# Optimization experiments

Measured on AMD Instinct MI355X. Metric: run time of the kernel, lower is better.

The kernel has to match this reference:

```python
import jax, jax.numpy as jnp
import numpy as np
import math

N_HEADS = 4
GELU = lambda x: jax.nn.gelu(x, approximate=False)  # torch nn.GELU default = exact erf

def _ln(x, s, b):
    m = jnp.mean(x, axis=-1, keepdims=True)
    v = jnp.mean((x - m) ** 2, axis=-1, keepdims=True)
    return (x - m) * jax.lax.rsqrt(v + 1e-5) * s + b

def _fwd(materials, in_seq, proj_vars, param_vars, enc_w1, enc_b1, enc_w2, enc_b2, sos,
         tl_wq, tl_wk, tl_wv, tl_bq, tl_bk, tl_bv, tl_wo, tl_bo,
         tl_ln1s, tl_ln1b, tl_ln2s, tl_ln2b, tl_fw1, tl_fb1, tl_fw2, tl_fb2,
         pw1, pb1, pw2, pb2, pw3, pb3, pw4, pb4, pw5, pb5,
         ipw1, ipb1, ipw2, ipb2, hw1, hb1, hw2, hb2, hw3, hb3):
    B = in_seq.shape[0]
    # encoder input MLP: [B,S,1] -> [B,S,D]
    x = GELU(in_seq @ enc_w1 + enc_b1) @ enc_w2 + enc_b2
    x = jnp.concatenate([jnp.broadcast_to(sos, (B, 1, sos.shape[-1])), x], axis=1)
    S1, D = x.shape[1], x.shape[2]
    dh = D // N_HEADS
    # sinusoidal positional encoding
    pos = jnp.arange(S1, dtype=jnp.float32)[:, None]
    div = jnp.exp(jnp.arange(0, D, 2, dtype=jnp.float32) * (-math.log(10000.0) / D))
    ang = pos * div
    pe = jnp.stack([jnp.sin(ang), jnp.cos(ang)], axis=-1).reshape(S1, D)
    x = x + pe
    scale = 1.0 / math.sqrt(dh)
    # post-LN TransformerEncoder layers (torch default norm_first=False), eval mode (no dropout)
    for l in range(tl_wq.shape[0]):
        q = (x @ tl_wq[l] + tl_bq[l]).reshape(B, S1, N_HEADS, dh).transpose(0, 2, 1, 3)
        k = (x @ tl_wk[l] + tl_bk[l]).reshape(B, S1, N_HEADS, dh).transpose(0, 2, 1, 3)
        v = (x @ tl_wv[l] + tl_bv[l]).reshape(B, S1, N_HEADS, dh).transpose(0, 2, 1, 3)
        att = jax.nn.softmax(jnp.einsum('bhqd,bhkd->bhqk', q, k) * scale, axis=-1)
        o = jnp.einsum('bhqk,bhkd->bhqd', att, v).transpose(0, 2, 1, 3).reshape(B, S1, D)
        x = _ln(x + o @ tl_wo[l] + tl_bo[l], tl_ln1s[l], tl_ln1b[l])
        f = GELU(x @ tl_fw1[l] + tl_fb1[l]) @ tl_fw2[l] + tl_fb2[l]
        x = _ln(x + f, tl_ln2s[l], tl_ln2b[l])
    sos_out = x[:, 0]
    h = jnp.concatenate([proj_vars, sos_out], axis=1)
    for w, b in ((pw1, pb1), (pw2, pb2), (pw3, pb3), (pw4, pb4)):
        h = GELU(h @ w + b)
    proj_out = h @ pw5 + pb5
    pp = GELU(param_vars @ ipw1 + ipb1) @ ipw2 + ipb2
    mi = jnp.concatenate([pp, proj_out], axis=1)  # [B, output_features+param_vars]
    # MaterialHead mask-gather-MLP-scatter == run every tiny head densely, pick by material id
    h1 = GELU(jnp.einsum('bi,mio->mbo', mi, hw1) + hb1[:, None, :])
    h2 = GELU(jnp.einsum('mbi,mio->mbo', h1, hw2) + hb2[:, None, :])
    h3 = jnp.einsum('mbi,mio->mbo', h2, hw3) + hb3[:, None, :]  # [M,B,1]
    return h3[materials, jnp.arange(B)]  # [B,1]

def setup_inputs() -> dict:
    key = jax.random.key(0)
    ks = iter(jax.random.split(key, 64))
    def rn(shape, scale=0.05):
        return jax.random.normal(next(ks), shape, dtype=jnp.float32) * scale
    B, S, IN, EL, D, L, DFF = 64, 1024, 1, 48, 64, 3, 256
    PV, PP, OF, M = 3, 3, 24, 3
    IF = OF + PP
    return dict(
        in_seq=rn((B, S, IN), 1.0),
        proj_vars=rn((B, PV), 1.0),
        param_vars=rn((B, PP), 1.0),
        materials=jax.random.randint(next(ks), (B,), 0, M),
        enc_w1=rn((IN, EL)), enc_b1=rn((EL,)), enc_w2=rn((EL, D)), enc_b2=rn((D,)),
        sos=rn((1, 1, D)),
        tl_wq=rn((L, D, D)), tl_wk=rn((L, D, D)), tl_wv=rn((L, D, D)),
        tl_bq=rn((L, D)), tl_bk=rn((L, D)), tl_bv=rn((L, D)),
        tl_wo=rn((L, D, D)), tl_bo=rn((L, D)),
        tl_ln1s=jnp.ones((L, D)), tl_ln1b=jnp.zeros((L, D)),
        tl_ln2s=jnp.ones((L, D)), tl_ln2b=jnp.zeros((L, D)),
        tl_fw1=rn((L, D, DFF)), tl_fb1=rn((L, DFF)), tl_fw2=rn((L, DFF, D)), tl_fb2=rn((L, D)),
        pw1=rn((PV + D, 34)), pb1=rn((34,)), pw2=rn((34, 11)), pb2=rn((11,)),
        pw3=rn((11, 36)), pb3=rn((36,)), pw4=rn((36, 22)), pb4=rn((22,)),
        pw5=rn((22, OF)), pb5=rn((OF,)),
        ipw1=rn((PP, 3)), ipb1=rn((3,)), ipw2=rn((3, PP)), ipb2=rn((PP,)),
        hw1=rn((M, IF, 15)), hb1=rn((M, 15)), hw2=rn((M, 15, 18)), hb2=rn((M, 18)),
        hw3=rn((M, 18, 1)), hb3=rn((M, 1)),
    )

def reference(in_seq, proj_vars, param_vars, materials, enc_w1, enc_b1, enc_w2, enc_b2, sos,
              tl_wq, tl_wk, tl_wv, tl_bq, tl_bk, tl_bv, tl_wo, tl_bo,
              tl_ln1s, tl_ln1b, tl_ln2s, tl_ln2b, tl_fw1, tl_fb1, tl_fw2, tl_fb2,
              pw1, pb1, pw2, pb2, pw3, pb3, pw4, pb4, pw5, pb5,
              ipw1, ipb1, ipw2, ipb2, hw1, hb1, hw2, hb2, hw3, hb3):
    return _fwd(materials, in_seq, proj_vars, param_vars, enc_w1, enc_b1, enc_w2, enc_b2, sos,
                tl_wq, tl_wk, tl_wv, tl_bq, tl_bk, tl_bv, tl_wo, tl_bo,
                tl_ln1s, tl_ln1b, tl_ln2s, tl_ln2b, tl_fw1, tl_fb1, tl_fw2, tl_fb2,
                pw1, pb1, pw2, pb2, pw3, pb3, pw4, pb4, pw5, pb5,
                ipw1, ipb1, ipw2, ipb2, hw1, hb1, hw2, hb2, hw3, hb3)
```

## Files before the change

kernel.cpp:

```cpp
#include <hip/hip_runtime.h>
#include <hip/hip_bf16.h>
#include <math.h>

#define BB   64
#define SS   1024
#define S1C  1025
#define DD   64
#define NHD  4
#define NBH  (BB * NHD)
#define DHD  16
#define DFFC 256
#define NLAY 3
#define NTOK (BB * S1C)
#define SPAD 1056
#define TGRP2 9
#define FTT   16
#define FT2   32
#define HPAD 264
#define OPAD 68
#define YPAD 72
#define QSCL 0.36067376022224085f

typedef const float* fp;
typedef __attribute__((ext_vector_type(8))) short bf16x8;
typedef __attribute__((ext_vector_type(4))) float f32x4;

#if __has_builtin(__builtin_amdgcn_exp2f)
#define RAW_EXP2(x) __builtin_amdgcn_exp2f(x)
#else
#define RAW_EXP2(x) __expf(0.6931471805599453f * (x))
#endif
#if __has_builtin(__builtin_amdgcn_rcpf)
#define RAW_RCP(x) __builtin_amdgcn_rcpf(x)
#else
#define RAW_RCP(x) (1.0f / (x))
#endif

__device__ __forceinline__ float gelu_exact(float x) {
    return 0.5f * x * (1.0f + erff(x * 0.7071067811865475f));
}
__device__ __forceinline__ float erf_fast(float x) {
    float ax = fabsf(x);
    float t = RAW_RCP(1.0f + 0.3275911f * ax);
    float p = t * (0.254829592f + t * (-0.284496736f + t * (1.421413741f +
              t * (-1.453152027f + t * 1.061405429f))));
    float e = RAW_EXP2(ax * ax * -1.4426950408889634f);
    float r = 1.0f - p * e;
    return copysignf(r, x);
}
__device__ __forceinline__ float gelu_fast(float x) {
    return 0.5f * x * (1.0f + erf_fast(x * 0.7071067811865475f));
}
__device__ __forceinline__ short f2b(float f) {
    unsigned u = __float_as_uint(f);
    return (short)((u + 0x7fffu + ((u >> 16) & 1u)) >> 16);
}
__device__ __forceinline__ short f2b_pos(float f) {
    return (short)((__float_as_uint(f) + 0x8000u) >> 16);
}

__global__ __launch_bounds__(256) void k_wconv(
    fp wq, fp wk, fp wv, fp wo, fp w1, fp w2,
    short* __restrict__ wqkvT, short* __restrict__ woT,
    short* __restrict__ w1T, short* __restrict__ w2T)
{
    int l = blockIdx.y;
    int i = blockIdx.x * 256 + threadIdx.x;
    if (i < 12288) {
        int p = i >> 12, rem = i & 4095;
        int d = rem >> 6, j = rem & 63;
        fp src = (p == 0 ? wq : p == 1 ? wk : wv) + (size_t)l * 4096;
        float v = src[j * 64 + d];
        if (p == 0) v *= QSCL;
        wqkvT[(size_t)l * 12288 + i] = f2b(v);
    } else if (i < 16384) {
        int rem = i - 12288;
        woT[(size_t)l * 4096 + rem] = f2b(wo[(size_t)l * 4096 + (rem & 63) * 64 + (rem >> 6)]);
    } else if (i < 32768) {
        int rem = i - 16384;
        w1T[(size_t)l * 16384 + rem] = f2b(w1[(size_t)l * 16384 + (rem & 63) * 256 + (rem >> 6)]);
    } else {
        int rem = i - 32768;
        w2T[(size_t)l * 16384 + rem] = f2b(w2[(size_t)l * 16384 + (rem & 255) * 64 + (rem >> 8)]);
    }
}

__global__ __launch_bounds__(64) void k_zero(
    short* __restrict__ qb, short* __restrict__ kb, short* __restrict__ vbt)
{
    int bh = blockIdx.x, t = threadIdx.x;
    for (int i = t; i < 31 * 16; i += 64) {
        int r = i >> 4, c = i & 15;
        size_t idx = ((size_t)bh * SPAD + 1025 + r) * 16 + c;
        qb[idx] = 0; kb[idx] = 0;
    }
    for (int i = t; i < 16 * 31; i += 64) {
        int e = i / 31, c = i % 31;
        vbt[((size_t)bh * 16 + e) * SPAD + 1025 + c] = 0;
    }
}

__global__ __launch_bounds__(256) void k_encode(
    fp in_seq, fp enc_w1, fp enc_b1, fp enc_w2, fp enc_b2, fp sos,
    float* __restrict__ x, short* __restrict__ xb)
{
    int t = threadIdx.x;
    int w = t >> 6, d = t & 63;
    int tok = blockIdx.x * 4 + w;
    int b = tok / S1C, s = tok % S1C;
    __shared__ float e[4][48];
    float val;
    if (s == 0) {
        val = sos[d];
    } else {
        float tin = in_seq[b * SS + (s - 1)];
        if (d < 48) e[w][d] = gelu_fast(tin * enc_w1[d] + enc_b1[d]);
        float acc = enc_b2[d];
        for (int j = 0; j < 48; ++j) acc += e[w][j] * enc_w2[j * DD + d];
        val = acc;
    }
    int i2 = (d >> 1) * 2;
    float factor = RAW_EXP2((float)i2 * (-9.210340371976184f / 64.0f) * 1.4426950408889634f);
    float ang = (float)s * factor;
    val += (d & 1) ? __cosf(ang) : __sinf(ang);
    x[(size_t)tok * DD + d] = val;
    xb[(size_t)tok * DD + d] = f2b(val);
}

__global__ __launch_bounds__(256) void k_qkv(
    const short* __restrict__ xb, const short* __restrict__ wqkvT,
    fp bq, fp bk, fp bv,
    short* __restrict__ qb, short* __restrict__ kb, short* __restrict__ vbt)
{
    int blk = blockIdx.x, t = threadIdx.x;
    int tok0 = blk * FTT;
    int w = t >> 6, l = t & 63;
    int quad = l >> 4, lo = l & 15;

    bf16x8 a0 = *(const bf16x8*)(xb + ((size_t)(tok0 + lo)) * DD + quad * 8);
    bf16x8 a1 = *(const bf16x8*)(xb + ((size_t)(tok0 + lo)) * DD + 32 + quad * 8);

    int tokr[4], br[4], sr[4];
    #pragma unroll
    for (int r = 0; r < 4; ++r) {
        tokr[r] = tok0 + quad * 4 + r;
        br[r] = tokr[r] / S1C; sr[r] = tokr[r] % S1C;
    }

    int n = w * 16 + lo;
    #pragma unroll
    for (int p = 0; p < 3; ++p) {
        const short* wT = wqkvT + (size_t)p * 4096 + (size_t)n * 64;
        bf16x8 b0 = *(const bf16x8*)(wT + quad * 8);
        bf16x8 b1 = *(const bf16x8*)(wT + 32 + quad * 8);
        f32x4 c = __builtin_amdgcn_mfma_f32_16x16x32_bf16(a0, b0, (f32x4){0,0,0,0}, 0, 0, 0);
        c = __builtin_amdgcn_mfma_f32_16x16x32_bf16(a1, b1, c, 0, 0, 0);
        float bias = (p == 0) ? bq[n] * QSCL : (p == 1) ? bk[n] : bv[n];
        #pragma unroll
        for (int r = 0; r < 4; ++r) {
            int bh = br[r] * NHD + w;
            short val = f2b(c[r] + bias);
            if (p == 0)      qb[((size_t)bh * SPAD + sr[r]) * 16 + lo] = val;
            else if (p == 1) kb[((size_t)bh * SPAD + sr[r]) * 16 + lo] = val;
            else             vbt[((size_t)bh * 16 + lo) * SPAD + sr[r]] = val;
        }
    }
}

__global__ __launch_bounds__(256) void k_attn(
    const short* __restrict__ qb, const short* __restrict__ kb,
    const short* __restrict__ vbt, short* __restrict__ ob)
{
    int bid = blockIdx.x;
    int bh  = bid % NBH;
    int grp = bid / NBH;
    int b = bh >> 2, h = bh & 3;
    int t = threadIdx.x;
    int w = t >> 6, l = t & 63;
    int quad = l >> 4, lo = l & 15;
    int t0 = grp * 4 + w;
    int t1 = t0 + 36;
    if (t1 > 65) t1 = 65;
    int qg0 = t0 * 16, qg1 = t1 * 16;

    __shared__ short pt_all[4][2][16][40];
    short (*pt0)[40] = pt_all[w][0];
    short (*pt1)[40] = pt_all[w][1];

    const short* qbase = qb + (size_t)bh * SPAD * 16;
    const short* kbase = kb + (size_t)bh * SPAD * 16;
    const short* vbase = vbt + (size_t)bh * 16 * SPAD;

    bf16x8 aQ0 = {0,0,0,0,0,0,0,0}, aQ1 = {0,0,0,0,0,0,0,0};
    if (quad < 2) {
        aQ0 = *(const bf16x8*)(qbase + ((size_t)(qg0 + lo)) * 16 + quad * 8);
        aQ1 = *(const bf16x8*)(qbase + ((size_t)(qg1 + lo)) * 16 + quad * 8);
    }

    const short ONE = 0x3F80;
    bf16x8 aOne = {ONE, ONE, ONE, ONE, ONE, ONE, ONE, ONE};

    f32x4 oc0 = {0.f,0.f,0.f,0.f}, oc1 = {0.f,0.f,0.f,0.f};
    f32x4 dn0 = {0.f,0.f,0.f,0.f}, dn1 = {0.f,0.f,0.f,0.f};

    for (int ch = 0; ch < 32; ++ch) {
        #pragma unroll
        for (int t01 = 0; t01 < 2; ++t01) {
            int krow = ch * 32 + t01 * 16 + lo;
            bf16x8 bK = *(const bf16x8*)(kbase + (size_t)krow * 16 + (quad & 1) * 8);
            f32x4 c0 = __builtin_amdgcn_mfma_f32_16x16x32_bf16(
                aQ0, bK, (f32x4){0.f,0.f,0.f,0.f}, 0, 0, 0);
            f32x4 c1 = __builtin_amdgcn_mfma_f32_16x16x32_bf16(
                aQ1, bK, (f32x4){0.f,0.f,0.f,0.f}, 0, 0, 0);
            #pragma unroll
            for (int r = 0; r < 4; ++r) {
                pt0[quad * 4 + r][t01 * 16 + lo] = f2b_pos(RAW_EXP2(c0[r]));
                pt1[quad * 4 + r][t01 * 16 + lo] = f2b_pos(RAW_EXP2(c1[r]));
            }
        }
        bf16x8 aV = *(const bf16x8*)(vbase + (size_t)lo * SPAD + ch * 32 + quad * 8);
        bf16x8 pB0 = *(const bf16x8*)&pt0[lo][quad * 8];
        oc0 = __builtin_amdgcn_mfma_f32_16x16x32_bf16(aV, pB0, oc0, 0, 0, 0);
        dn0 = __builtin_amdgcn_mfma_f32_16x16x32_bf16(aOne, pB0, dn0, 0, 0, 0);
        bf16x8 pB1 = *(const bf16x8*)&pt1[lo][quad * 8];
        oc1 = __builtin_amdgcn_mfma_f32_16x16x32_bf16(aV, pB1, oc1, 0, 0, 0);
        dn1 = __builtin_amdgcn_mfma_f32_16x16x32_bf16(aOne, pB1, dn1, 0, 0, 0);
    }
    {
        #pragma unroll
        for (int t01 = 0; t01 < 2; ++t01) {
            int krow = 1024 + t01 * 16 + lo;
            bf16x8 bK = *(const bf16x8*)(kbase + (size_t)krow * 16 + (quad & 1) * 8);
            f32x4 c0 = __builtin_amdgcn_mfma_f32_16x16x32_bf16(
                aQ0, bK, (f32x4){0.f,0.f,0.f,0.f}, 0, 0, 0);
            f32x4 c1 = __builtin_amdgcn_mfma_f32_16x16x32_bf16(
                aQ1, bK, (f32x4){0.f,0.f,0.f,0.f}, 0, 0, 0);
            bool valid = (krow <= 1024);
            #pragma unroll
            for (int r = 0; r < 4; ++r) {
                pt0[quad * 4 + r][t01 * 16 + lo] = f2b_pos(valid ? RAW_EXP2(c0[r]) : 0.f);
                pt1[quad * 4 + r][t01 * 16 + lo] = f2b_pos(valid ? RAW_EXP2(c1[r]) : 0.f);
            }
        }
        bf16x8 aV = *(const bf16x8*)(vbase + (size_t)lo * SPAD + 1024 + quad * 8);
        bf16x8 pB0 = *(const bf16x8*)&pt0[lo][quad * 8];
        oc0 = __builtin_amdgcn_mfma_f32_16x16x32_bf16(aV, pB0, oc0, 0, 0, 0);
        dn0 = __builtin_amdgcn_mfma_f32_16x16x32_bf16(aOne, pB0, dn0, 0, 0, 0);
        bf16x8 pB1 = *(const bf16x8*)&pt1[lo][quad * 8];
        oc1 = __builtin_amdgcn_mfma_f32_16x16x32_bf16(aV, pB1, oc1, 0, 0, 0);
        dn1 = __builtin_amdgcn_mfma_f32_16x16x32_bf16(aOne, pB1, dn1, 0, 0, 0);
    }

    {
        int qrow = qg0 + lo;
        if (qrow < S1C) {
            float inv = 1.0f / dn0[0];
            unsigned p0 = (unsigned short)f2b(oc0[0] * inv) | ((unsigned)(unsigned short)f2b(oc0[1] * inv) << 16);
            unsigned p1 = (unsigned short)f2b(oc0[2] * inv) | ((unsigned)(unsigned short)f2b(oc0[3] * inv) << 16);
            *(uint2*)(ob + ((size_t)b * S1C + qrow) * DD + h * DHD + quad * 4) = make_uint2(p0, p1);
        }
    }
    {
        int qrow = qg1 + lo;
        if (qrow < S1C) {
            float inv = 1.0f / dn1[0];
            unsigned p0 = (unsigned short)f2b(oc1[0] * inv) | ((unsigned)(unsigned short)f2b(oc1[1] * inv) << 16);
            unsigned p1 = (unsigned short)f2b(oc1[2] * inv) | ((unsigned)(unsigned short)f2b(oc1[3] * inv) << 16);
            *(uint2*)(ob + ((size_t)b * S1C + qrow) * DD + h * DHD + quad * 4) = make_uint2(p0, p1);
        }
    }
}

__global__ __launch_bounds__(256) void k_block(
    const short* __restrict__ ob, float* __restrict__ x,
    const short* __restrict__ woT, fp bo, fp ln1s, fp ln1b,
    const short* __restrict__ w1T, fp b1, const short* __restrict__ w2T, fp b2,
    fp ln2s, fp ln2b,
    const short* __restrict__ wqkvTn, fp bqn, fp bkn, fp bvn,
    short* __restrict__ qb, short* __restrict__ kb, short* __restrict__ vbt,
    int has_next)
{
    int blk = blockIdx.x, t = threadIdx.x;
    int tok0 = blk * FT2;
    int w = t >> 6, l = t & 63;
    int quad = l >> 4, lo = l & 15;

    __shared__ float otf[FT2][OPAD];
    __shared__ short ys[FT2][YPAD];
    __shared__ short hid[FT2][HPAD];

    {
        const short* obp0 = ob + ((size_t)(tok0 + lo)) * DD;
        const short* obp1 = ob + ((size_t)(tok0 + 16 + lo)) * DD;
        bf16x8 a0 = *(const bf16x8*)(obp0 + quad * 8);
        bf16x8 a1 = *(const bf16x8*)(obp0 + 32 + quad * 8);
        bf16x8 a2 = *(const bf16x8*)(obp1 + quad * 8);
        bf16x8 a3 = *(const bf16x8*)(obp1 + 32 + quad * 8);
        int n = w * 16 + lo;
        const short* wT = woT + (size_t)n * 64;
        bf16x8 b0 = *(const bf16x8*)(wT + quad * 8);
        bf16x8 bb = *(const bf16x8*)(wT + 32 + quad * 8);
        f32x4 c0 = __builtin_amdgcn_mfma_f32_16x16x32_bf16(a0, b0, (f32x4){0,0,0,0}, 0, 0, 0);
        c0 = __builtin_amdgcn_mfma_f32_16x16x32_bf16(a1, bb, c0, 0, 0, 0);
        f32x4 c1 = __builtin_amdgcn_mfma_f32_16x16x32_bf16(a2, b0, (f32x4){0,0,0,0}, 0, 0, 0);
        c1 = __builtin_amdgcn_mfma_f32_16x16x32_bf16(a3, bb, c1, 0, 0, 0);
        float bov = bo[n];
        #pragma unroll
        for (int r = 0; r < 4; ++r) {
            otf[quad * 4 + r][n] = c0[r] + bov;
            otf[16 + quad * 4 + r][n] = c1[r] + bov;
        }
    }
    __syncthreads();

    int d = l;
    float yv[8];
    {
        float s1 = ln1s[d], bl1 = ln1b[d];
        #pragma unroll
        for (int i = 0; i < 8; ++i) {
            int tt = w * 8 + i;
            float val = otf[tt][d] + x[(size_t)(tok0 + tt) * DD + d];
            float sum = val, vs = val * val;
            #pragma unroll
            for (int off = 32; off > 0; off >>= 1) {
                sum += __shfl_xor(sum, off, 64);
                vs  += __shfl_xor(vs, off, 64);
            }
            float mean = sum * (1.0f / 64.0f);
            float var = vs * (1.0f / 64.0f) - mean * mean;
            float y = (val - mean) * rsqrtf(var + 1e-5f) * s1 + bl1;
            yv[i] = y;
            ys[tt][d] = f2b(y);
        }
    }
    __syncthreads();

    {
        bf16x8 a0 = *(const bf16x8*)&ys[lo][quad * 8];
        bf16x8 a1 = *(const bf16x8*)&ys[lo][32 + quad * 8];
        bf16x8 a2 = *(const bf16x8*)&ys[16 + lo][quad * 8];
        bf16x8 a3 = *(const bf16x8*)&ys[16 + lo][32 + quad * 8];
        #pragma unroll
        for (int i = 0; i < 4; ++i) {
            int n = w * 64 + i * 16 + lo;
            const short* wT = w1T + (size_t)n * 64;
            bf16x8 b0 = *(const bf16x8*)(wT + quad * 8);
            bf16x8 bb = *(const bf16x8*)(wT + 32 + quad * 8);
            f32x4 c0 = __builtin_amdgcn_mfma_f32_16x16x32_bf16(a0, b0, (f32x4){0,0,0,0}, 0, 0, 0);
            c0 = __builtin_amdgcn_mfma_f32_16x16x32_bf16(a1, bb, c0, 0, 0, 0);
            f32x4 c1 = __builtin_amdgcn_mfma_f32_16x16x32_bf16(a2, b0, (f32x4){0,0,0,0}, 0, 0, 0);
            c1 = __builtin_amdgcn_mfma_f32_16x16x32_bf16(a3, bb, c1, 0, 0, 0);
            float b1v = b1[n];
            #pragma unroll
            for (int r = 0; r < 4; ++r) {
                hid[quad * 4 + r][n] = f2b(gelu_fast(c0[r] + b1v));
                hid[16 + quad * 4 + r][n] = f2b(gelu_fast(c1[r] + b1v));
            }
        }
    }
    __syncthreads();

    {
        f32x4 c20 = {0.f,0.f,0.f,0.f}, c21 = {0.f,0.f,0.f,0.f};
        const short* wT2 = w2T + (size_t)(w * 16 + lo) * 256;
        #pragma unroll
        for (int kc = 0; kc < 8; ++kc) {
            bf16x8 b2f = *(const bf16x8*)(wT2 + kc * 32 + quad * 8);
            bf16x8 a20 = *(const bf16x8*)&hid[lo][kc * 32 + quad * 8];
            bf16x8 a21 = *(const bf16x8*)&hid[16 + lo][kc * 32 + quad * 8];
            c20 = __builtin_amdgcn_mfma_f32_16x16x32_bf16(a20, b2f, c20, 0, 0, 0);
            c21 = __builtin_amdgcn_mfma_f32_16x16x32_bf16(a21, b2f, c21, 0, 0, 0);
        }
        float b2v = b2[w * 16 + lo];
        #pragma unroll
        for (int r = 0; r < 4; ++r) {
            otf[quad * 4 + r][w * 16 + lo] = c20[r] + b2v;
            otf[16 + quad * 4 + r][w * 16 + lo] = c21[r] + b2v;
        }
    }
    __syncthreads();

    {
        float s2 = ln2s[d], bl2 = ln2b[d];
        #pragma unroll
        for (int i = 0; i < 8; ++i) {
            int tt = w * 8 + i;
            float val = otf[tt][d] + yv[i];
            float sum = val, vs = val * val;
            #pragma unroll
            for (int off = 32; off > 0; off >>= 1) {
                sum += __shfl_xor(sum, off, 64);
                vs  += __shfl_xor(vs, off, 64);
            }
            float mean = sum * (1.0f / 64.0f);
            float var = vs * (1.0f / 64.0f) - mean * mean;
            float y = (val - mean) * rsqrtf(var + 1e-5f) * s2 + bl2;
            x[(size_t)(tok0 + tt) * DD + d] = y;
            ys[tt][d] = f2b(y);
        }
    }
    __syncthreads();

    if (has_next) {
        bf16x8 a0 = *(const bf16x8*)&ys[lo][quad * 8];
        bf16x8 a1 = *(const bf16x8*)&ys[lo][32 + quad * 8];
        bf16x8 a2 = *(const bf16x8*)&ys[16 + lo][quad * 8];
        bf16x8 a3 = *(const bf16x8*)&ys[16 + lo][32 + quad * 8];
        int n = w * 16 + lo;
        #pragma unroll
        for (int p = 0; p < 3; ++p) {
            const short* wT = wqkvTn + (size_t)p * 4096 + (size_t)n * 64;
            bf16x8 b0 = *(const bf16x8*)(wT + quad * 8);
            bf16x8 bb = *(const bf16x8*)(wT + 32 + quad * 8);
            f32x4 c0 = __builtin_amdgcn_mfma_f32_16x16x32_bf16(a0, b0, (f32x4){0,0,0,0}, 0, 0, 0);
            c0 = __builtin_amdgcn_mfma_f32_16x16x32_bf16(a1, bb, c0, 0, 0, 0);
            f32x4 c1 = __builtin_amdgcn_mfma_f32_16x16x32_bf16(a2, b0, (f32x4){0,0,0,0}, 0, 0, 0);
            c1 = __builtin_amdgcn_mfma_f32_16x16x32_bf16(a3, bb, c1, 0, 0, 0);
            float bias = (p == 0) ? bqn[n] * QSCL : (p == 1) ? bkn[n] : bvn[n];
            #pragma unroll
            for (int r = 0; r < 4; ++r) {
                int tok = tok0 + quad * 4 + r;
                int bb0 = tok / S1C, ss0 = tok % S1C;
                int bh = bb0 * NHD + w;
                short val = f2b(c0[r] + bias);
                int tok2 = tok + 16;
                int bb1 = tok2 / S1C, ss1 = tok2 % S1C;
                int bh2 = bb1 * NHD + w;
                short val2 = f2b(c1[r] + bias);
                if (p == 0) {
                    qb[((size_t)bh * SPAD + ss0) * 16 + lo] = val;
                    qb[((size_t)bh2 * SPAD + ss1) * 16 + lo] = val2;
                } else if (p == 1) {
                    kb[((size_t)bh * SPAD + ss0) * 16 + lo] = val;
                    kb[((size_t)bh2 * SPAD + ss1) * 16 + lo] = val2;
                } else {
                    vbt[((size_t)bh * 16 + lo) * SPAD + ss0] = val;
                    vbt[((size_t)bh2 * 16 + lo) * SPAD + ss1] = val2;
                }
            }
        }
    }
}

__global__ __launch_bounds__(64) void k_head(
    const float* __restrict__ x, fp proj_vars, fp param_vars,
    const int* __restrict__ materials,
    fp pw1, fp pb1, fp pw2, fp pb2, fp pw3, fp pb3,
    fp pw4, fp pb4, fp pw5, fp pb5,
    fp ipw1, fp ipb1, fp ipw2, fp ipb2,
    fp hw1, fp hb1, fp hw2, fp hb2, fp hw3, fp hb3,
    float* __restrict__ out)
{
    int b = blockIdx.x;
    int tid = threadIdx.x;
    __shared__ float A[80], Bf[80], pp[8], mi[32];

    if (tid < 3) A[tid] = proj_vars[b * 3 + tid];
    A[3 + tid] = x[((size_t)b * S1C + 0) * DD + tid];
    __syncthreads();

    if (tid < 34) {
        float a = pb1[tid];
        for (int i = 0; i < 67; ++i) a += A[i] * pw1[i * 34 + tid];
        Bf[tid] = gelu_exact(a);
    }
    __syncthreads();
    if (tid < 11) {
        float a = pb2[tid];
        for (int i = 0; i < 34; ++i) a += Bf[i] * pw2[i * 11 + tid];
        A[tid] = gelu_exact(a);
    }
    __syncthreads();
    if (tid < 36) {
        float a = pb3[tid];
        for (int i = 0; i < 11; ++i) a += A[i] * pw3[i * 36 + tid];
        Bf[tid] = gelu_exact(a);
    }
    __syncthreads();
    if (tid < 22) {
        float a = pb4[tid];
        for (int i = 0; i < 36; ++i) a += Bf[i] * pw4[i * 22 + tid];
        A[tid] = gelu_exact(a);
    }
    __syncthreads();
    if (tid < 24) {
        float a = pb5[tid];
        for (int i = 0; i < 22; ++i) a += A[i] * pw5[i * 24 + tid];
        mi[3 + tid] = a;
    }
    if (tid < 3) {
        float a = ipb1[tid];
        for (int i = 0; i < 3; ++i) a += param_vars[b * 3 + i] * ipw1[i * 3 + tid];
        pp[tid] = gelu_exact(a);
    }
    __syncthreads();
    if (tid < 3) {
        float a = ipb2[tid];
        for (int i = 0; i < 3; ++i) a += pp[i] * ipw2[i * 3 + tid];
        mi[tid] = a;
    }
    __syncthreads();

    int m = materials[b];
    if (tid < 15) {
        float a = hb1[m * 15 + tid];
        for (int i = 0; i < 27; ++i) a += mi[i] * hw1[(m * 27 + i) * 15 + tid];
        A[tid] = gelu_exact(a);
    }
    __syncthreads();
    if (tid < 18) {
        float a = hb2[m * 18 + tid];
        for (int i = 0; i < 15; ++i) a += A[i] * hw2[(m * 15 + i) * 18 + tid];
        Bf[tid] = gelu_exact(a);
    }
    __syncthreads();
    if (tid == 0) {
        float a = hb3[m];
        for (int i = 0; i < 18; ++i) a += Bf[i] * hw3[m * 18 + i];
        out[b] = a;
    }
}

extern "C" void kernel_launch(void* const* d_in, const int* in_sizes, int n_in,
                              void* d_out, int out_size, void* d_ws, size_t ws_size,
                              hipStream_t stream) {
    fp in_seq     = (fp)d_in[0];
    fp proj_vars  = (fp)d_in[1];
    fp param_vars = (fp)d_in[2];
    const int* materials = (const int*)d_in[3];
    fp enc_w1 = (fp)d_in[4];
    fp enc_b1 = (fp)d_in[5];
    fp enc_w2 = (fp)d_in[6];
    fp enc_b2 = (fp)d_in[7];
    fp sos    = (fp)d_in[8];
    fp tl_wq  = (fp)d_in[9];
    fp tl_wk  = (fp)d_in[10];
    fp tl_wv  = (fp)d_in[11];
    fp tl_bq  = (fp)d_in[12];
    fp tl_bk  = (fp)d_in[13];
    fp tl_bv  = (fp)d_in[14];
    fp tl_wo  = (fp)d_in[15];
    fp tl_bo  = (fp)d_in[16];
    fp tl_ln1s = (fp)d_in[17];
    fp tl_ln1b = (fp)d_in[18];
    fp tl_ln2s = (fp)d_in[19];
    fp tl_ln2b = (fp)d_in[20];
    fp tl_fw1 = (fp)d_in[21];
    fp tl_fb1 = (fp)d_in[22];
    fp tl_fw2 = (fp)d_in[23];
    fp tl_fb2 = (fp)d_in[24];
    fp pw1 = (fp)d_in[25]; fp pb1 = (fp)d_in[26];
    fp pw2 = (fp)d_in[27]; fp pb2 = (fp)d_in[28];
    fp pw3 = (fp)d_in[29]; fp pb3 = (fp)d_in[30];
    fp pw4 = (fp)d_in[31]; fp pb4 = (fp)d_in[32];
    fp pw5 = (fp)d_in[33]; fp pb5 = (fp)d_in[34];
    fp ipw1 = (fp)d_in[35]; fp ipb1 = (fp)d_in[36];
    fp ipw2 = (fp)d_in[37]; fp ipb2 = (fp)d_in[38];
    fp hw1 = (fp)d_in[39]; fp hb1 = (fp)d_in[40];
    fp hw2 = (fp)d_in[41]; fp hb2 = (fp)d_in[42];
    fp hw3 = (fp)d_in[43]; fp hb3 = (fp)d_in[44];

    float* x  = (float*)d_ws;
    short* ob = (short*)(x + (size_t)NTOK * DD);
    short* xb = ob + (size_t)NTOK * DD;
    short* qb = xb + (size_t)NTOK * DD;
    short* kb = qb + (size_t)NBH * SPAD * 16;
    short* vbt = kb + (size_t)NBH * SPAD * 16;
    short* wqkvT = vbt + (size_t)NBH * 16 * SPAD;
    short* woT = wqkvT + (size_t)NLAY * 12288;
    short* w1T = woT + (size_t)NLAY * 4096;
    short* w2T = w1T + (size_t)NLAY * 16384;

    k_wconv<<<dim3(192, NLAY), 256, 0, stream>>>(
        tl_wq, tl_wk, tl_wv, tl_wo, tl_fw1, tl_fw2, wqkvT, woT, w1T, w2T);
    k_zero<<<NBH, 64, 0, stream>>>(qb, kb, vbt);
    k_encode<<<NTOK / 4, 256, 0, stream>>>(in_seq, enc_w1, enc_b1, enc_w2, enc_b2, sos, x, xb);

    k_qkv<<<NTOK / FTT, 256, 0, stream>>>(
        xb, wqkvT,
        tl_bq, tl_bk, tl_bv,
        qb, kb, vbt);

    for (int l = 0; l < NLAY; ++l) {
        k_attn<<<NBH * TGRP2, 256, 0, stream>>>(qb, kb, vbt, ob);
        int ln = (l + 1 < NLAY) ? (l + 1) : l;
        k_block<<<NTOK / FT2, 256, 0, stream>>>(
            ob, x,
            woT + (size_t)l * 4096, tl_bo + (size_t)l * DD,
            tl_ln1s + (size_t)l * DD, tl_ln1b + (size_t)l * DD,
            w1T + (size_t)l * 16384, tl_fb1 + (size_t)l * DFFC,
            w2T + (size_t)l * 16384, tl_fb2 + (size_t)l * DD,
            tl_ln2s + (size_t)l * DD, tl_ln2b + (size_t)l * DD,
            wqkvT + (size_t)ln * 12288,
            tl_bq + (size_t)ln * DD, tl_bk + (size_t)ln * DD, tl_bv + (size_t)ln * DD,
            qb, kb, vbt,
            (l + 1 < NLAY) ? 1 : 0);
    }

    k_head<<<BB, 64, 0, stream>>>(
        x, proj_vars, param_vars, materials,
        pw1, pb1, pw2, pb2, pw3, pb3, pw4, pb4, pw5, pb5,
        ipw1, ipb1, ipw2, ipb2,
        hw1, hb1, hw2, hb2, hw3, hb3,
        (float*)d_out);
}
```

Measured before the change: 530.0 us.

## Restructure attention to register-only 16x16x16 MFMA with transposed score layout

The attention kernel now computes K·Qᵀ so the exponentiated score tile comes out directly in the B-operand layout of the following P·V MFMA. This removes the shared-memory round trip for probabilities, and the 16x16x16 bf16 MFMA avoids zero-padding the 16-wide head dimension to 32. Each wave now handles three query tiles instead of two, and the grid shrinks from 9 to 6 groups per batch-head, which amortises K/V loads over more queries. In exchange, the kernel issues more, smaller MFMAs and each wave holds more registers.

```diff
diff --git a/kernel.cpp b/kernel.cpp
--- a/kernel.cpp
+++ b/kernel.cpp
@@ -13,7 +13,6 @@
 #define NLAY 3
 #define NTOK (BB * S1C)
 #define SPAD 1056
-#define TGRP2 9
 #define FTT   16
 #define FT2   32
 #define HPAD 264
@@ -23,6 +22,7 @@
 
 typedef const float* fp;
 typedef __attribute__((ext_vector_type(8))) short bf16x8;
+typedef __attribute__((ext_vector_type(4))) short bf16x4;
 typedef __attribute__((ext_vector_type(4))) float f32x4;
 
 #if __has_builtin(__builtin_amdgcn_exp2f)
@@ -36,6 +36,16 @@
 #define RAW_RCP(x) (1.0f / (x))
 #endif
 
+__device__ __forceinline__ f32x4 mfma16(bf16x4 a, bf16x4 b, f32x4 c) {
+#if __has_builtin(__builtin_amdgcn_mfma_f32_16x16x16bf16_1k)
+    return __builtin_amdgcn_mfma_f32_16x16x16bf16_1k(a, b, c, 0, 0, 0);
+#else
+    bf16x8 az = {a[0], a[1], a[2], a[3], 0, 0, 0, 0};
+    bf16x8 bz = {b[0], b[1], b[2], b[3], 0, 0, 0, 0};
+    return __builtin_amdgcn_mfma_f32_16x16x32_bf16(az, bz, c, 0, 0, 0);
+#endif
+}
+
 __device__ __forceinline__ float gelu_exact(float x) {
     return 0.5f * x * (1.0f + erff(x * 0.7071067811865475f));
 }
@@ -57,6 +67,16 @@
 }
 __device__ __forceinline__ short f2b_pos(float f) {
     return (short)((__float_as_uint(f) + 0x8000u) >> 16);
+}
+__device__ __forceinline__ bf16x4 exppack(f32x4 c) {
+    unsigned e0 = __float_as_uint(RAW_EXP2(c[0]));
+    unsigned e1 = __float_as_uint(RAW_EXP2(c[1]));
+    unsigned e2 = __float_as_uint(RAW_EXP2(c[2]));
+    unsigned e3 = __float_as_uint(RAW_EXP2(c[3]));
+    unsigned u01 = ((e0 + 0x8000u) >> 16) | ((e1 + 0x8000u) & 0xffff0000u);
+    unsigned u23 = ((e2 + 0x8000u) >> 16) | ((e3 + 0x8000u) & 0xffff0000u);
+    uint2 uu = make_uint2(u01, u23);
+    return __builtin_bit_cast(bf16x4, uu);
 }
 
 __global__ __launch_bounds__(256) void k_wconv(
@@ -173,82 +193,60 @@
 {
     int bid = blockIdx.x;
     int bh  = bid % NBH;
-    int grp = bid / NBH;
+    int g   = bid / NBH;
     int b = bh >> 2, h = bh & 3;
     int t = threadIdx.x;
     int w = t >> 6, l = t & 63;
     int quad = l >> 4, lo = l & 15;
-    int t0 = grp * 4 + w;
-    int t1 = t0 + 36;
-    if (t1 > 65) t1 = 65;
-    int qg0 = t0 * 16, qg1 = t1 * 16;
-
-    __shared__ short pt_all[4][2][16][40];
-    short (*pt0)[40] = pt_all[w][0];
-    short (*pt1)[40] = pt_all[w][1];
+    int s = g * 4 + w;
+    int t0 = s, t1 = s + 24, t2 = s + 48;
+    if (t2 > 65) t2 = 65;
+    int qg0 = t0 * 16, qg1 = t1 * 16, qg2 = t2 * 16;
 
     const short* qbase = qb + (size_t)bh * SPAD * 16;
     const short* kbase = kb + (size_t)bh * SPAD * 16;
     const short* vbase = vbt + (size_t)bh * 16 * SPAD;
 
-    bf16x8 aQ0 = {0,0,0,0,0,0,0,0}, aQ1 = {0,0,0,0,0,0,0,0};
-    if (quad < 2) {
-        aQ0 = *(const bf16x8*)(qbase + ((size_t)(qg0 + lo)) * 16 + quad * 8);
-        aQ1 = *(const bf16x8*)(qbase + ((size_t)(qg1 + lo)) * 16 + quad * 8);
-    }
+    bf16x4 aQ0 = *(const bf16x4*)(qbase + ((size_t)(qg0 + lo)) * 16 + quad * 4);
+    bf16x4 aQ1 = *(const bf16x4*)(qbase + ((size_t)(qg1 + lo)) * 16 + quad * 4);
+    bf16x4 aQ2 = *(const bf16x4*)(qbase + ((size_t)(qg2 + lo)) * 16 + quad * 4);
 
     const short ONE = 0x3F80;
-    bf16x8 aOne = {ONE, ONE, ONE, ONE, ONE, ONE, ONE, ONE};
-
-    f32x4 oc0 = {0.f,0.f,0.f,0.f}, oc1 = {0.f,0.f,0.f,0.f};
-    f32x4 dn0 = {0.f,0.f,0.f,0.f}, dn1 = {0.f,0.f,0.f,0.f};
-
-    for (int ch = 0; ch < 32; ++ch) {
-        #pragma unroll
-        for (int t01 = 0; t01 < 2; ++t01) {
-            int krow = ch * 32 + t01 * 16 + lo;
-            bf16x8 bK = *(const bf16x8*)(kbase + (size_t)krow * 16 + (quad & 1) * 8);
-            f32x4 c0 = __builtin_amdgcn_mfma_f32_16x16x32_bf16(
-                aQ0, bK, (f32x4){0.f,0.f,0.f,0.f}, 0, 0, 0);
-            f32x4 c1 = __builtin_amdgcn_mfma_f32_16x16x32_bf16(
-                aQ1, bK, (f32x4){0.f,0.f,0.f,0.f}, 0, 0, 0);
-            #pragma unroll
-            for (int r = 0; r < 4; ++r) {
-                pt0[quad * 4 + r][t01 * 16 + lo] = f2b_pos(RAW_EXP2(c0[r]));
-                pt1[quad * 4 + r][t01 * 16 + lo] = f2b_pos(RAW_EXP2(c1[r]));
-            }
-        }
-        bf16x8 aV = *(const bf16x8*)(vbase + (size_t)lo * SPAD + ch * 32 + quad * 8);
-        bf16x8 pB0 = *(const bf16x8*)&pt0[lo][quad * 8];
-        oc0 = __builtin_amdgcn_mfma_f32_16x16x32_bf16(aV, pB0, oc0, 0, 0, 0);
-        dn0 = __builtin_amdgcn_mfma_f32_16x16x32_bf16(aOne, pB0, dn0, 0, 0, 0);
-        bf16x8 pB1 = *(const bf16x8*)&pt1[lo][quad * 8];
-        oc1 = __builtin_amdgcn_mfma_f32_16x16x32_bf16(aV, pB1, oc1, 0, 0, 0);
-        dn1 = __builtin_amdgcn_mfma_f32_16x16x32_bf16(aOne, pB1, dn1, 0, 0, 0);
-    }
-    {
-        #pragma unroll
-        for (int t01 = 0; t01 < 2; ++t01) {
-            int krow = 1024 + t01 * 16 + lo;
-            bf16x8 bK = *(const bf16x8*)(kbase + (size_t)krow * 16 + (quad & 1) * 8);
-            f32x4 c0 = __builtin_amdgcn_mfma_f32_16x16x32_bf16(
-                aQ0, bK, (f32x4){0.f,0.f,0.f,0.f}, 0, 0, 0);
-            f32x4 c1 = __builtin_amdgcn_mfma_f32_16x16x32_bf16(
-                aQ1, bK, (f32x4){0.f,0.f,0.f,0.f}, 0, 0, 0);
-            bool valid = (krow <= 1024);
-            #pragma unroll
-            for (int r = 0; r < 4; ++r) {
-                pt0[quad * 4 + r][t01 * 16 + lo] = f2b_pos(valid ? RAW_EXP2(c0[r]) : 0.f);
-                pt1[quad * 4 + r][t01 * 16 + lo] = f2b_pos(valid ? RAW_EXP2(c1[r]) : 0.f);
-            }
-        }
-        bf16x8 aV = *(const bf16x8*)(vbase + (size_t)lo * SPAD + 1024 + quad * 8);
-        bf16x8 pB0 = *(const bf16x8*)&pt0[lo][quad * 8];
-        oc0 = __builtin_amdgcn_mfma_f32_16x16x32_bf16(aV, pB0, oc0, 0, 0, 0);
-        dn0 = __builtin_amdgcn_mfma_f32_16x16x32_bf16(aOne, pB0, dn0, 0, 0, 0);
-        bf16x8 pB1 = *(const bf16x8*)&pt1[lo][quad * 8];
-        oc1 = __builtin_amdgcn_mfma_f32_16x16x32_bf16(aV, pB1, oc1, 0, 0, 0);
-        dn1 = __builtin_amdgcn_mfma_f32_16x16x32_bf16(aOne, pB1, dn1, 0, 0, 0);
+    bf16x4 aOne = {ONE, ONE, ONE, ONE};
+    const f32x4 Z = {0.f, 0.f, 0.f, 0.f};
+
+    f32x4 oc0 = Z, oc1 = Z, oc2 = Z;
+    f32x4 dn0 = Z, dn1 = Z, dn2 = Z;
+
+    #pragma unroll 4
+    for (int ch = 0; ch < 64; ++ch) {
+        bf16x4 aK = *(const bf16x4*)(kbase + ((size_t)(ch * 16 + lo)) * 16 + quad * 4);
+        bf16x4 aV = *(const bf16x4*)(vbase + (size_t)lo * SPAD + ch * 16 + quad * 4);
+        f32x4 c0 = mfma16(aK, aQ0, Z);
+        f32x4 c1 = mfma16(aK, aQ1, Z);
+        f32x4 c2 = mfma16(aK, aQ2, Z);
+        bf16x4 p0 = exppack(c0);
+        bf16x4 p1 = exppack(c1);
+        bf16x4 p2 = exppack(c2);
+        oc0 = mfma16(aV, p0, oc0);  dn0 = mfma16(aOne, p0, dn0);
+        oc1 = mfma16(aV, p1, oc1);  dn1 = mfma16(aOne, p1, dn1);
+        oc2 = mfma16(aV, p2, oc2);  dn2 = mfma16(aOne, p2, dn2);
+    }
+    {
+        bf16x4 aK = *(const bf16x4*)(kbase + ((size_t)(1024 + lo)) * 16 + quad * 4);
+        bf16x4 aV = *(const bf16x4*)(vbase + (size_t)lo * SPAD + 1024 + quad * 4);
+        f32x4 c0 = mfma16(aK, aQ0, Z);
+        f32x4 c1 = mfma16(aK, aQ1, Z);
+        f32x4 c2 = mfma16(aK, aQ2, Z);
+        unsigned m0 = (quad == 0) ? ((__float_as_uint(RAW_EXP2(c0[0])) + 0x8000u) >> 16) : 0u;
+        unsigned m1 = (quad == 0) ? ((__float_as_uint(RAW_EXP2(c1[0])) + 0x8000u) >> 16) : 0u;
+        unsigned m2 = (quad == 0) ? ((__float_as_uint(RAW_EXP2(c2[0])) + 0x8000u) >> 16) : 0u;
+        bf16x4 p0 = __builtin_bit_cast(bf16x4, make_uint2(m0, 0u));
+        bf16x4 p1 = __builtin_bit_cast(bf16x4, make_uint2(m1, 0u));
+        bf16x4 p2 = __builtin_bit_cast(bf16x4, make_uint2(m2, 0u));
+        oc0 = mfma16(aV, p0, oc0);  dn0 = mfma16(aOne, p0, dn0);
+        oc1 = mfma16(aV, p1, oc1);  dn1 = mfma16(aOne, p1, dn1);
+        oc2 = mfma16(aV, p2, oc2);  dn2 = mfma16(aOne, p2, dn2);
     }
 
     {
@@ -266,6 +264,15 @@
             float inv = 1.0f / dn1[0];
             unsigned p0 = (unsigned short)f2b(oc1[0] * inv) | ((unsigned)(unsigned short)f2b(oc1[1] * inv) << 16);
             unsigned p1 = (unsigned short)f2b(oc1[2] * inv) | ((unsigned)(unsigned short)f2b(oc1[3] * inv) << 16);
+            *(uint2*)(ob + ((size_t)b * S1C + qrow) * DD + h * DHD + quad * 4) = make_uint2(p0, p1);
+        }
+    }
+    {
+        int qrow = qg2 + lo;
+        if (qrow < S1C) {
+            float inv = 1.0f / dn2[0];
+            unsigned p0 = (unsigned short)f2b(oc2[0] * inv) | ((unsigned)(unsigned short)f2b(oc2[1] * inv) << 16);
+            unsigned p1 = (unsigned short)f2b(oc2[2] * inv) | ((unsigned)(unsigned short)f2b(oc2[3] * inv) << 16);
             *(uint2*)(ob + ((size_t)b * S1C + qrow) * DD + h * DHD + quad * 4) = make_uint2(p0, p1);
         }
     }
@@ -583,7 +590,7 @@
         qb, kb, vbt);
 
     for (int l = 0; l < NLAY; ++l) {
-        k_attn<<<NBH * TGRP2, 256, 0, stream>>>(qb, kb, vbt, ob);
+        k_attn<<<NBH * 6, 256, 0, stream>>>(qb, kb, vbt, ob);
         int ln = (l + 1 < NLAY) ? (l + 1) : l;
         k_block<<<NTOK / FT2, 256, 0, stream>>>(
             ob, x,
```

New measurement: 547.9 us. 1.03x slower.
